# Kernel tuning notes

Hardware: AMD Instinct MI355X
Metric: run time of the kernel (lower is better)

Reference implementation:

```python
import jax, jax.numpy as jnp
import numpy as np
import math

D = 768      # embedding_dim
H = 12       # attn_n_heads
HD = D // H  # head_dim = 64
F = 3072     # ff_latent_dim
B, S = 1, 4096
EPS = 1e-5


def setup_inputs() -> dict:
    key = jax.random.key(0)
    ks = jax.random.split(key, 16)
    s = 0.02
    return {
        "x": jax.random.normal(ks[0], (B, S, D), jnp.float32),
        # per-head Q/K/V projections stacked: [H, D, HD]
        "Wq": jax.random.normal(ks[1], (H, D, HD), jnp.float32) * s,
        "bq": jnp.zeros((H, HD), jnp.float32),
        "Wk": jax.random.normal(ks[2], (H, D, HD), jnp.float32) * s,
        "bk": jnp.zeros((H, HD), jnp.float32),
        "Wv": jax.random.normal(ks[3], (H, D, HD), jnp.float32) * s,
        "bv": jnp.zeros((H, HD), jnp.float32),
        "Wo": jax.random.normal(ks[4], (D, D), jnp.float32) * s,
        "bo": jnp.zeros((D,), jnp.float32),
        "ln1_w": jnp.ones((D,), jnp.float32),
        "ln1_b": jnp.zeros((D,), jnp.float32),
        "ln2_w": jnp.ones((D,), jnp.float32),
        "ln2_b": jnp.zeros((D,), jnp.float32),
        "W1": jax.random.normal(ks[5], (D, F), jnp.float32) * s,
        "b1": jnp.zeros((F,), jnp.float32),
        "W2": jax.random.normal(ks[6], (F, D), jnp.float32) * s,
        "b2": jnp.zeros((D,), jnp.float32),
    }


def _layer_norm(z, w, b):
    mu = jnp.mean(z, axis=-1, keepdims=True)
    var = jnp.mean(jnp.square(z - mu), axis=-1, keepdims=True)
    return (z - mu) * jax.lax.rsqrt(var + EPS) * w + b


def reference(x, Wq, bq, Wk, bk, Wv, bv, Wo, bo,
              ln1_w, ln1_b, ln2_w, ln2_b, W1, b1, W2, b2):
    # pre-norm attention block
    y = _layer_norm(x, ln1_w, ln1_b)
    q = jnp.einsum('bsd,hde->bhse', y, Wq) + bq[None, :, None, :]
    k = jnp.einsum('bsd,hde->bhse', y, Wk) + bk[None, :, None, :]
    v = jnp.einsum('bsd,hde->bhse', y, Wv) + bv[None, :, None, :]
    scores = jnp.einsum('bhqe,bhke->bhqk', q, k) * (1.0 / math.sqrt(HD))
    attn = jax.nn.softmax(scores, axis=-1)            # [B,H,S,S]
    o = jnp.einsum('bhqk,bhke->bhqe', attn, v)        # [B,H,S,HD]
    o = o.transpose(0, 2, 1, 3).reshape(x.shape[0], x.shape[1], D)  # concat heads
    o = o @ Wo + bo
    x = x + o
    # pre-norm FFN block (eval mode: dropout is identity)
    y = _layer_norm(x, ln2_w, ln2_b)
    h = jax.nn.gelu(y @ W1 + b1, approximate=False)   # torch F.gelu default = exact erf
    x = x + (h @ W2 + b2)
    return x
```

## Files before the change

### kernel.cpp

```cpp
#include <hip/hip_runtime.h>
#include <stdint.h>

typedef __bf16 bf16;
typedef __bf16 bf16x2 __attribute__((ext_vector_type(2)));
typedef __bf16 bf16x4 __attribute__((ext_vector_type(4)));
typedef __bf16 bf16x8 __attribute__((ext_vector_type(8)));
typedef float f32x4 __attribute__((ext_vector_type(4)));
typedef float f32x16 __attribute__((ext_vector_type(16)));
typedef uint32_t u32;
typedef unsigned int u32x2 __attribute__((ext_vector_type(2)));

#define QSCALE 0.1803368801111137f

__device__ __forceinline__ float fast_exp2(float x) {
#if __has_builtin(__builtin_amdgcn_exp2f)
  return __builtin_amdgcn_exp2f(x);
#else
  return exp2f(x);
#endif
}

__device__ __forceinline__ float fast_rcp(float x) {
#if __has_builtin(__builtin_amdgcn_rcpf)
  return __builtin_amdgcn_rcpf(x);
#else
  return 1.0f / x;
#endif
}

__device__ __forceinline__ float fast_gelu(float v) {
  float u = v * 0.70710678118654752f;
  float a = __builtin_fabsf(u);
  float t = fast_rcp(__builtin_fmaf(0.47047f, a, 1.0f));
  float e = fast_exp2(-a * a * 1.4426950408889634f);
  float poly = ((0.7478556f * t - 0.0958798f) * t + 0.3480242f) * t;
  float erf_abs = __builtin_fmaf(-poly, e, 1.0f);
  float erf = __builtin_copysignf(erf_abs, u);
  return 0.5f * v * (1.0f + erf);
}

__device__ __forceinline__ u32 pack_bf16(float a, float b) {
  bf16x2 v; v[0] = (bf16)a; v[1] = (bf16)b;
  return __builtin_bit_cast(u32, v);
}

__device__ __forceinline__ void permswap32(u32& a, u32& b) {
#if __has_builtin(__builtin_amdgcn_permlane32_swap)
  u32x2 r = __builtin_amdgcn_permlane32_swap(a, b, false, false);
  a = r[0]; b = r[1];
#else
  asm volatile("v_permlane32_swap_b32 %0, %1" : "+v"(a), "+v"(b));
#endif
}

__device__ __forceinline__ void async16(void* lds, const void* g) {
  __builtin_amdgcn_global_load_lds(
      (__attribute__((address_space(1))) uint32_t*)(uintptr_t)g,
      (__attribute__((address_space(3))) uint32_t*)(uint32_t)(uintptr_t)lds,
      16, 0, 0);
}

__device__ __forceinline__ void transpose_body(
    const float* __restrict__ in, bf16* __restrict__ outp, int R, int C,
    int bx, int by, float (*tile)[33], int t)
{
  int bc = bx * 32, br = by * 32;
  int tc = t & 31, tr = t >> 5;
  #pragma unroll
  for (int i = 0; i < 4; i++)
    tile[tr + i * 8][tc] = in[(size_t)(br + tr + i * 8) * C + bc + tc];
  __syncthreads();
  #pragma unroll
  for (int i = 0; i < 4; i++) {
    int c = bc + tr + i * 8;
    outp[(size_t)c * R + br + tc] = (bf16)tile[tc][tr + i * 8];
  }
}

__global__ __launch_bounds__(256) void prep_kernel(
    const float* __restrict__ x,
    const float* __restrict__ ln1w, const float* __restrict__ ln1b,
    const float* __restrict__ Wq, const float* __restrict__ Wk,
    const float* __restrict__ Wv,
    const float* __restrict__ Wo, const float* __restrict__ W1,
    const float* __restrict__ W2,
    const float* __restrict__ bq, const float* __restrict__ bk,
    const float* __restrict__ bv,
    bf16* __restrict__ ybuf, bf16* __restrict__ Wqkv_t,
    bf16* __restrict__ Wo_t, bf16* __restrict__ W1_t, bf16* __restrict__ W2_t,
    float* __restrict__ bqkv)
{
  __shared__ float tile[32][33];
  int n = blockIdx.x;
  int t = threadIdx.x;
  if (n < 4096) {
    int row = n;
    const float* xr = x + (size_t)row * 768;
    float v0 = xr[t], v1 = xr[t + 256], v2 = xr[t + 512];
    float s = v0 + v1 + v2, s2 = v0 * v0 + v1 * v1 + v2 * v2;
    #pragma unroll
    for (int d = 1; d < 64; d <<= 1) {
      s  += __shfl_xor(s, d, 64);
      s2 += __shfl_xor(s2, d, 64);
    }
    float* red = &tile[0][0];
    int wv = t >> 6, ln = t & 63;
    if (ln == 0) { red[wv] = s; red[4 + wv] = s2; }
    __syncthreads();
    s  = red[0] + red[1] + red[2] + red[3];
    s2 = red[4] + red[5] + red[6] + red[7];
    float mu = s * (1.0f / 768.0f);
    float var = s2 * (1.0f / 768.0f) - mu * mu;
    float rstd = rsqrtf(var + 1e-5f);
    bf16* yr = ybuf + (size_t)row * 768;
    yr[t]       = (bf16)((v0 - mu) * rstd * ln1w[t]       + ln1b[t]);
    yr[t + 256] = (bf16)((v1 - mu) * rstd * ln1w[t + 256] + ln1b[t + 256]);
    yr[t + 512] = (bf16)((v2 - mu) * rstd * ln1w[t + 512] + ln1b[t + 512]);
  } else if (n < 5824) {
    int n2 = n - 4096;
    int bz = n2 / 48, rem = n2 - bz * 48;
    int by = rem / 24, bx = rem - by * 24;
    int part = bz / 12, h = bz - part * 12;
    const float* W = (part == 0) ? Wq : (part == 1) ? Wk : Wv;
    float sc = (part == 0) ? QSCALE : 1.0f;
    int bd = bx * 32, be = by * 32;
    int tc = t & 31, tr = t >> 5;
    #pragma unroll
    for (int i = 0; i < 4; i++)
      tile[tr + i * 8][tc] = W[((size_t)h * 768 + bd + tr + i * 8) * 64 + be + tc] * sc;
    __syncthreads();
    #pragma unroll
    for (int i = 0; i < 4; i++) {
      int e = be + tr + i * 8;
      Wqkv_t[(size_t)(part * 768 + h * 64 + e) * 768 + bd + tc] = (bf16)tile[tc][tr + i * 8];
    }
  } else if (n < 6400) {
    int m = n - 5824;
    transpose_body(Wo, Wo_t, 768, 768, m % 24, m / 24, tile, t);
  } else if (n < 8704) {
    int m = n - 6400;
    transpose_body(W1, W1_t, 768, 3072, m % 96, m / 96, tile, t);
  } else if (n < 11008) {
    int m = n - 8704;
    transpose_body(W2, W2_t, 3072, 768, m % 24, m / 24, tile, t);
  } else {
    int idx = (n - 11008) * 256 + t;
    int part = idx / 768, nn = idx - part * 768;
    const float* B = (part == 0) ? bq : (part == 1) ? bk : bv;
    float v = B[nn];
    if (part == 0) v *= QSCALE;
    bqkv[idx] = v;
  }
}

__global__ __launch_bounds__(256) void reduce_add2_kernel(
    float* __restrict__ out, const bf16* __restrict__ p1,
    const bf16* __restrict__ p2)
{
  int i = blockIdx.x * 256 + threadIdx.x;
  float4 o = ((float4*)out)[i];
  bf16x4 a = ((const bf16x4*)p1)[i];
  bf16x4 b = ((const bf16x4*)p2)[i];
  o.x += (float)a[0] + (float)b[0];
  o.y += (float)a[1] + (float)b[1];
  o.z += (float)a[2] + (float)b[2];
  o.w += (float)a[3] + (float)b[3];
  ((float4*)out)[i] = o;
}

__global__ __launch_bounds__(256) void ln_add_kernel(
    float* __restrict__ x1, const bf16* __restrict__ p,
    const float* __restrict__ w, const float* __restrict__ b,
    bf16* __restrict__ y)
{
  int row = blockIdx.x;
  float* xr = x1 + (size_t)row * 768;
  const bf16* pr = p + (size_t)row * 768;
  int t = threadIdx.x;
  float v0 = xr[t]       + (float)pr[t];
  float v1 = xr[t + 256] + (float)pr[t + 256];
  float v2 = xr[t + 512] + (float)pr[t + 512];
  xr[t] = v0; xr[t + 256] = v1; xr[t + 512] = v2;
  float s = v0 + v1 + v2, s2 = v0 * v0 + v1 * v1 + v2 * v2;
  #pragma unroll
  for (int d = 1; d < 64; d <<= 1) {
    s  += __shfl_xor(s, d, 64);
    s2 += __shfl_xor(s2, d, 64);
  }
  __shared__ float red[8];
  int wv = t >> 6, ln = t & 63;
  if (ln == 0) { red[wv] = s; red[4 + wv] = s2; }
  __syncthreads();
  s  = red[0] + red[1] + red[2] + red[3];
  s2 = red[4] + red[5] + red[6] + red[7];
  float mu = s * (1.0f / 768.0f);
  float var = s2 * (1.0f / 768.0f) - mu * mu;
  float rstd = rsqrtf(var + 1e-5f);
  bf16* yr = y + (size_t)row * 768;
  yr[t]       = (bf16)((v0 - mu) * rstd * w[t]       + b[t]);
  yr[t + 256] = (bf16)((v1 - mu) * rstd * w[t + 256] + b[t + 256]);
  yr[t + 512] = (bf16)((v2 - mu) * rstd * w[t + 512] + b[t + 512]);
}

template <int MODE>
__global__ __launch_bounds__(256) void gemm_bt(
    const bf16* __restrict__ A, const bf16* __restrict__ Bt,
    const float* __restrict__ bias, const float* __restrict__ res,
    void* __restrict__ outp, void* __restrict__ out2, int M, int N, int K)
{
  __shared__ bf16 As[2 * 128 * 32];
  __shared__ bf16 Bs[2 * 128 * 32];
  int t = threadIdx.x;
  int w = t >> 6, lane = t & 63;
  int quad = lane >> 4, l16 = lane & 15;
  int tile_m = blockIdx.y * 128, tile_n = blockIdx.x * 128;

  int srow = lane >> 2;
  int skb = (lane & 3) * 8;
  const bf16* Ag = A  + (size_t)(tile_m + w * 16 + srow) * K + skb;
  const bf16* Bg = Bt + (size_t)(tile_n + w * 16 + srow) * K + skb;
  char* AsB = (char*)As + w * 1024;
  char* BsB = (char*)Bs + w * 1024;
  size_t rstep = (size_t)64 * K;

  int wm = (w >> 1) * 64, wn = (w & 1) * 64;
  f32x4 acc[4][4] = {};

  int kbeg = 0, kend = K;
  if (MODE == 5) {
    int slice = K / (int)gridDim.z;
    kbeg = blockIdx.z * slice;
    kend = kbeg + slice;
  }

  async16(AsB,        Ag + kbeg);
  async16(AsB + 4096, Ag + rstep + kbeg);
  async16(BsB,        Bg + kbeg);
  async16(BsB + 4096, Bg + rstep + kbeg);

  int cur = 0;
  for (int k0 = kbeg; k0 < kend; k0 += 32) {
    __syncthreads();
    if (k0 + 32 < kend) {
      char* An = AsB + (cur ^ 1) * 8192;
      char* Bn = BsB + (cur ^ 1) * 8192;
      async16(An,        Ag + k0 + 32);
      async16(An + 4096, Ag + rstep + k0 + 32);
      async16(Bn,        Bg + k0 + 32);
      async16(Bn + 4096, Bg + rstep + k0 + 32);
    }
    const bf16* Ab = As + cur * 4096;
    const bf16* Bb = Bs + cur * 4096;

    bf16x8 af[4], bfr[4];
    #pragma unroll
    for (int mb = 0; mb < 4; mb++)
      af[mb] = *(const bf16x8*)(Ab + (wm + mb * 16 + l16) * 32 + quad * 8);
    #pragma unroll
    for (int nb = 0; nb < 4; nb++)
      bfr[nb] = *(const bf16x8*)(Bb + (wn + nb * 16 + l16) * 32 + quad * 8);
    #pragma unroll
    for (int mb = 0; mb < 4; mb++)
      #pragma unroll
      for (int nb = 0; nb < 4; nb++)
        acc[mb][nb] = __builtin_amdgcn_mfma_f32_16x16x32_bf16(
            af[mb], bfr[nb], acc[mb][nb], 0, 0, 0);
    cur ^= 1;
  }

  #pragma unroll
  for (int mb = 0; mb < 4; mb++) {
    #pragma unroll
    for (int nb = 0; nb < 4; nb++) {
      int col = tile_n + wn + nb * 16 + l16;
      int row0 = tile_m + wm + mb * 16 + quad * 4;
      if (MODE == 4) {
        float bc = bias[col];
        if (col < 1536) {
          #pragma unroll
          for (int r = 0; r < 4; r++)
            ((bf16*)outp)[(size_t)(row0 + r) * 1536 + col] =
                (bf16)(acc[mb][nb][r] + bc);
        } else {
          bf16x4 pk;
          #pragma unroll
          for (int r = 0; r < 4; r++) pk[r] = (bf16)(acc[mb][nb][r] + bc);
          *(bf16x4*)((bf16*)out2 + (size_t)(col - 1536) * 4096 + row0) = pk;
        }
      } else if (MODE == 2) {
        float bc = bias[col];
        #pragma unroll
        for (int r = 0; r < 4; r++) {
          size_t idx = (size_t)(row0 + r) * N + col;
          ((bf16*)outp)[idx] = (bf16)fast_gelu(acc[mb][nb][r] + bc);
        }
      } else {
        if (blockIdx.z == 0) {
          float bc = bias[col];
          #pragma unroll
          for (int r = 0; r < 4; r++) {
            size_t idx = (size_t)(row0 + r) * N + col;
            ((float*)outp)[idx] = res[idx] + acc[mb][nb][r] + bc;
          }
        } else {
          size_t pbase = (size_t)(blockIdx.z - 1) * M * N;
          #pragma unroll
          for (int r = 0; r < 4; r++) {
            size_t idx = (size_t)(row0 + r) * N + col;
            ((bf16*)out2)[pbase + idx] = (bf16)acc[mb][nb][r];
          }
        }
      }
    }
  }
}

__global__ __launch_bounds__(256) void flash_kernel(
    const bf16* __restrict__ qk, const bf16* __restrict__ vtg,
    bf16* __restrict__ Opart, float* __restrict__ Lpart)
{
  __shared__ char smem[49152];
  bf16* Qs = (bf16*)smem;
  int t = threadIdx.x, w = t >> 6, lane = t & 63;
  int l32 = lane & 31, hi = lane >> 5;
  int qt = blockIdx.x, h = blockIdx.y, z = blockIdx.z;
  int q0 = qt * 128, kv0 = z * 2048;
  int qsel = w & 1, ksel = w >> 1;
  int qw = qsel * 64, kb = ksel * 32;

  int srow = lane >> 3, scol = ((lane & 7) ^ srow) * 8;

  #pragma unroll
  for (int c = 0; c < 4; c++) {
    const bf16* qg = qk + (size_t)(q0 + c * 32 + w * 8 + srow) * 1536 + h * 64 + scol;
    async16(smem + c * 4096 + w * 1024, qg);
  }

  const bf16* kg = qk + 768 + h * 64 + (size_t)(kv0 + w * 8 + srow) * 1536 + scol;
  const bf16* vg = vtg + (size_t)(h * 64 + w * 8 + srow) * 4096 + kv0 + scol;

  {
    char* kb0 = smem + 16384 + w * 1024;
    char* vb0 = smem + 32768 + w * 1024;
    async16(kb0,        kg);
    async16(kb0 + 4096, kg + (size_t)32 * 1536);
    async16(vb0,        vg);
    async16(vb0 + 4096, vg + (size_t)32 * 4096);
  }
  __syncthreads();

  int qr0 = qw + l32, qr1 = qw + 32 + l32;
  bf16x8 qf0[4], qf1[4];
  #pragma unroll
  for (int ks = 0; ks < 4; ks++) {
    qf0[ks] = *(const bf16x8*)(Qs + qr0 * 64 + (((ks * 2 + hi) ^ (qr0 & 7)) * 8));
    qf1[ks] = *(const bf16x8*)(Qs + qr1 * 64 + (((ks * 2 + hi) ^ (qr1 & 7)) * 8));
  }

  f32x16 oT00 = {}, oT10 = {}, oT01 = {}, oT11 = {};
  float l0 = 0.0f, l1 = 0.0f;
  int krow = kb + l32;
  int er0 = l32, er1 = 32 + l32;

  for (int j = 0; j < 32; j++) {
    int cur = j & 1;
    if (j < 31) {
      const bf16* kgn = kg + (size_t)(j + 1) * 64 * 1536;
      const bf16* vgn = vg + (j + 1) * 64;
      char* kbn = smem + 16384 + (cur ^ 1) * 8192 + w * 1024;
      char* vbn = smem + 32768 + (cur ^ 1) * 8192 + w * 1024;
      async16(kbn,        kgn);
      async16(kbn + 4096, kgn + (size_t)32 * 1536);
      async16(vbn,        vgn);
      async16(vbn + 4096, vgn + (size_t)32 * 4096);
    }
    const bf16* Ks = (const bf16*)(smem + 16384 + cur * 8192);
    const bf16* Vs = (const bf16*)(smem + 32768 + cur * 8192);

    f32x16 s0 = {}, s1 = {};
    __builtin_amdgcn_s_setprio(1);
    #pragma unroll
    for (int ks = 0; ks < 4; ks++) {
      bf16x8 kf = *(const bf16x8*)(Ks + krow * 64 + (((ks * 2 + hi) ^ (krow & 7)) * 8));
      s0 = __builtin_amdgcn_mfma_f32_32x32x16_bf16(kf, qf0[ks], s0, 0, 0, 0);
      s1 = __builtin_amdgcn_mfma_f32_32x32x16_bf16(kf, qf1[ks], s1, 0, 0, 0);
    }
    __builtin_amdgcn_s_setprio(0);

    bf16x8 pf00, pf01, pf10, pf11;
    {
      float p[16];
      #pragma unroll
      for (int i = 0; i < 16; i++) p[i] = fast_exp2(s0[i]);
      float t0 = (p[0] + p[1]) + (p[2] + p[3]);
      float t1 = (p[4] + p[5]) + (p[6] + p[7]);
      float t2 = (p[8] + p[9]) + (p[10] + p[11]);
      float t3 = (p[12] + p[13]) + (p[14] + p[15]);
      l0 += (t0 + t1) + (t2 + t3);
      u32 dd[8];
      #pragma unroll
      for (int k = 0; k < 8; k++) dd[k] = pack_bf16(p[2 * k], p[2 * k + 1]);
      permswap32(dd[0], dd[2]);
      permswap32(dd[1], dd[3]);
      permswap32(dd[4], dd[6]);
      permswap32(dd[5], dd[7]);
      pf00 = __builtin_bit_cast(bf16x8, uint4{dd[0], dd[1], dd[2], dd[3]});
      pf01 = __builtin_bit_cast(bf16x8, uint4{dd[4], dd[5], dd[6], dd[7]});
    }
    {
      float p[16];
      #pragma unroll
      for (int i = 0; i < 16; i++) p[i] = fast_exp2(s1[i]);
      float t0 = (p[0] + p[1]) + (p[2] + p[3]);
      float t1 = (p[4] + p[5]) + (p[6] + p[7]);
      float t2 = (p[8] + p[9]) + (p[10] + p[11]);
      float t3 = (p[12] + p[13]) + (p[14] + p[15]);
      l1 += (t0 + t1) + (t2 + t3);
      u32 dd[8];
      #pragma unroll
      for (int k = 0; k < 8; k++) dd[k] = pack_bf16(p[2 * k], p[2 * k + 1]);
      permswap32(dd[0], dd[2]);
      permswap32(dd[1], dd[3]);
      permswap32(dd[4], dd[6]);
      permswap32(dd[5], dd[7]);
      pf10 = __builtin_bit_cast(bf16x8, uint4{dd[0], dd[1], dd[2], dd[3]});
      pf11 = __builtin_bit_cast(bf16x8, uint4{dd[4], dd[5], dd[6], dd[7]});
    }

    __builtin_amdgcn_s_setprio(1);
    #pragma unroll
    for (int kstep = 0; kstep < 2; kstep++) {
      int grp = (kb >> 3) + kstep * 2 + hi;
      bf16x8 va = *(const bf16x8*)(Vs + er0 * 64 + ((grp ^ (er0 & 7)) * 8));
      bf16x8 vb = *(const bf16x8*)(Vs + er1 * 64 + ((grp ^ (er1 & 7)) * 8));
      bf16x8 pa = kstep ? pf01 : pf00;
      bf16x8 pb = kstep ? pf11 : pf10;
      oT00 = __builtin_amdgcn_mfma_f32_32x32x16_bf16(va, pa, oT00, 0, 0, 0);
      oT10 = __builtin_amdgcn_mfma_f32_32x32x16_bf16(vb, pa, oT10, 0, 0, 0);
      oT01 = __builtin_amdgcn_mfma_f32_32x32x16_bf16(va, pb, oT01, 0, 0, 0);
      oT11 = __builtin_amdgcn_mfma_f32_32x32x16_bf16(vb, pb, oT11, 0, 0, 0);
    }
    __builtin_amdgcn_s_setprio(0);

    __syncthreads();
  }

  float lq0 = l0 + __shfl_xor(l0, 32, 64);
  float lq1 = l1 + __shfl_xor(l1, 32, 64);
  float* OS = (float*)smem;
  float* LS = (float*)(smem + 34304);
  if (ksel == 1) {
    #pragma unroll
    for (int i = 0; i < 16; i++) {
      int eoff = (i & 3) + 8 * (i >> 2) + 4 * hi;
      OS[qr0 * 67 + eoff]      = oT00[i];
      OS[qr0 * 67 + 32 + eoff] = oT10[i];
      OS[qr1 * 67 + eoff]      = oT01[i];
      OS[qr1 * 67 + 32 + eoff] = oT11[i];
    }
    if (hi == 0) { LS[qr0] = lq0; LS[qr1] = lq1; }
  }
  __syncthreads();
  if (ksel == 0) {
    size_t tb = ((size_t)z * 12 + h) * 32 + qt;
    float la0 = lq0 + LS[qr0], la1 = lq1 + LS[qr1];
    if (hi == 0) { Lpart[tb * 128 + qr0] = la0; Lpart[tb * 128 + qr1] = la1; }
    bf16* ob0 = Opart + tb * 8192 + (size_t)qr0 * 64;
    bf16* ob1 = Opart + tb * 8192 + (size_t)qr1 * 64;
    #pragma unroll
    for (int g = 0; g < 4; g++) {
      int e0 = 8 * g + 4 * hi;
      bf16x4 a0, a1, b0, b1;
      #pragma unroll
      for (int r = 0; r < 4; r++) {
        a0[r] = (bf16)(oT00[g * 4 + r] + OS[qr0 * 67 + e0 + r]);
        a1[r] = (bf16)(oT10[g * 4 + r] + OS[qr0 * 67 + 32 + e0 + r]);
        b0[r] = (bf16)(oT01[g * 4 + r] + OS[qr1 * 67 + e0 + r]);
        b1[r] = (bf16)(oT11[g * 4 + r] + OS[qr1 * 67 + 32 + e0 + r]);
      }
      *(bf16x4*)(ob0 + e0)      = a0;
      *(bf16x4*)(ob0 + 32 + e0) = a1;
      *(bf16x4*)(ob1 + e0)      = b0;
      *(bf16x4*)(ob1 + 32 + e0) = b1;
    }
  }
}

__global__ __launch_bounds__(256) void flash_combine_kernel(
    const bf16* __restrict__ Opart, const float* __restrict__ Lpart,
    bf16* __restrict__ o)
{
  int qt = blockIdx.x, h = blockIdx.y;
  int t = threadIdx.x;
  size_t t0 = (size_t)h * 32 + qt;
  size_t t1 = (size_t)(12 + h) * 32 + qt;
  #pragma unroll
  for (int qq = 0; qq < 2; qq++) {
    int q = qq * 64 + (t >> 2), eg = (t & 3) * 16;
    float inv = 1.0f / (Lpart[t0 * 128 + q] + Lpart[t1 * 128 + q]);
    const bf16* p0 = Opart + t0 * 8192 + (size_t)q * 64 + eg;
    const bf16* p1 = Opart + t1 * 8192 + (size_t)q * 64 + eg;
    bf16x8 a0 = *(const bf16x8*)p0, a1 = *(const bf16x8*)(p0 + 8);
    bf16x8 b0 = *(const bf16x8*)p1, b1 = *(const bf16x8*)(p1 + 8);
    bf16x8 r0, r1;
    #pragma unroll
    for (int i = 0; i < 8; i++) {
      r0[i] = (bf16)(((float)a0[i] + (float)b0[i]) * inv);
      r1[i] = (bf16)(((float)a1[i] + (float)b1[i]) * inv);
    }
    bf16* op = o + (size_t)(qt * 128 + q) * 768 + h * 64 + eg;
    *(bf16x8*)op       = r0;
    *(bf16x8*)(op + 8) = r1;
  }
}

extern "C" void kernel_launch(void* const* d_in, const int* in_sizes, int n_in,
                              void* d_out, int out_size, void* d_ws, size_t ws_size,
                              hipStream_t stream) {
  const float* x    = (const float*)d_in[0];
  const float* Wq   = (const float*)d_in[1];
  const float* bq   = (const float*)d_in[2];
  const float* Wk   = (const float*)d_in[3];
  const float* bk   = (const float*)d_in[4];
  const float* Wv   = (const float*)d_in[5];
  const float* bv   = (const float*)d_in[6];
  const float* Wo   = (const float*)d_in[7];
  const float* bo   = (const float*)d_in[8];
  const float* ln1w = (const float*)d_in[9];
  const float* ln1b = (const float*)d_in[10];
  const float* ln2w = (const float*)d_in[11];
  const float* ln2b = (const float*)d_in[12];
  const float* W1   = (const float*)d_in[13];
  const float* b1   = (const float*)d_in[14];
  const float* W2   = (const float*)d_in[15];
  const float* b2   = (const float*)d_in[16];
  float* out = (float*)d_out;

  char* ws = (char*)d_ws;
  bf16*  hbuf   = (bf16*)(ws + 0);
  float* Lpart  = (float*)(ws + 0);
  bf16*  ybuf   = (bf16*)(ws + 0);
  bf16*  qkbuf  = (bf16*)(ws + 6291456);
  bf16*  opar_o = (bf16*)(ws + 6291456);
  bf16*  vtg    = (bf16*)(ws + 18874368);
  float* x1     = (float*)(ws + 25165824);
  bf16*  Opart  = (bf16*)(ws + 25165824);
  bf16*  obuf   = (bf16*)(ws + 37748736);
  bf16*  y2buf  = obuf;
  bf16*  opar_f = obuf;
  bf16*  Wqkv_t = (bf16*)(ws + 44040192);
  bf16*  Wo_t   = (bf16*)(ws + 47579136);
  bf16*  W1_t   = (bf16*)(ws + 48758784);
  bf16*  W2_t   = (bf16*)(ws + 53477376);
  float* bqkv   = (float*)(ws + 58195968);

  prep_kernel<<<11017, 256, 0, stream>>>(x, ln1w, ln1b, Wq, Wk, Wv, Wo, W1, W2,
                                         bq, bk, bv,
                                         ybuf, Wqkv_t, Wo_t, W1_t, W2_t, bqkv);
  gemm_bt<4><<<dim3(18, 32), 256, 0, stream>>>(ybuf, Wqkv_t, bqkv,
                                               (const float*)nullptr, qkbuf, vtg,
                                               4096, 2304, 768);
  flash_kernel<<<dim3(32, 12, 2), 256, 0, stream>>>(qkbuf, vtg, Opart, Lpart);
  flash_combine_kernel<<<dim3(32, 12), 256, 0, stream>>>(Opart, Lpart, obuf);
  gemm_bt<5><<<dim3(6, 32, 2), 256, 0, stream>>>(obuf, Wo_t, bo, x, x1, opar_o,
                                                 4096, 768, 768);
  ln_add_kernel<<<4096, 256, 0, stream>>>(x1, opar_o, ln2w, ln2b, y2buf);
  gemm_bt<2><<<dim3(24, 32), 256, 0, stream>>>(y2buf, W1_t, b1,
                                               (const float*)nullptr, hbuf, nullptr,
                                               4096, 3072, 768);
  gemm_bt<5><<<dim3(6, 32, 3), 256, 0, stream>>>(hbuf, W2_t, b2, x1, out, opar_f,
                                                 4096, 768, 3072);
  reduce_add2_kernel<<<3072, 256, 0, stream>>>(out, opar_f,
                                               (const bf16*)(ws + 44040192));
}
```

Baseline: 315.2 us.

## Split flash attention KV into three chunks and halve shared memory

Result: no change. 313.9 us (-0.4%).

```diff
diff --git a/kernel.cpp b/kernel.cpp
--- a/kernel.cpp
+++ b/kernel.cpp
@@ -153,18 +153,14 @@
   }
 }
 
-__global__ __launch_bounds__(256) void reduce_add2_kernel(
-    float* __restrict__ out, const bf16* __restrict__ p1,
-    const bf16* __restrict__ p2)
+__global__ __launch_bounds__(256) void reduce_add_kernel(
+    float* __restrict__ out, const bf16* __restrict__ p)
 {
   int i = blockIdx.x * 256 + threadIdx.x;
   float4 o = ((float4*)out)[i];
-  bf16x4 a = ((const bf16x4*)p1)[i];
-  bf16x4 b = ((const bf16x4*)p2)[i];
-  o.x += (float)a[0] + (float)b[0];
-  o.y += (float)a[1] + (float)b[1];
-  o.z += (float)a[2] + (float)b[2];
-  o.w += (float)a[3] + (float)b[3];
+  bf16x4 v = ((const bf16x4*)p)[i];
+  o.x += (float)v[0]; o.y += (float)v[1];
+  o.z += (float)v[2]; o.w += (float)v[3];
   ((float4*)out)[i] = o;
 }
 
@@ -317,14 +313,15 @@
 
 __global__ __launch_bounds__(256) void flash_kernel(
     const bf16* __restrict__ qk, const bf16* __restrict__ vtg,
-    bf16* __restrict__ Opart, float* __restrict__ Lpart)
+    bf16* __restrict__ Op0, bf16* __restrict__ Op12, float* __restrict__ Lpart)
 {
-  __shared__ char smem[49152];
-  bf16* Qs = (bf16*)smem;
+  __shared__ char smem[32768];
   int t = threadIdx.x, w = t >> 6, lane = t & 63;
   int l32 = lane & 31, hi = lane >> 5;
   int qt = blockIdx.x, h = blockIdx.y, z = blockIdx.z;
-  int q0 = qt * 128, kv0 = z * 2048;
+  int q0 = qt * 128;
+  int nt  = (z == 0) ? 22 : 21;
+  int kv0 = (z == 0) ? 0 : (22 + (z - 1) * 21) * 64;
   int qsel = w & 1, ksel = w >> 1;
   int qw = qsel * 64, kb = ksel * 32;
 
@@ -333,15 +330,16 @@
   #pragma unroll
   for (int c = 0; c < 4; c++) {
     const bf16* qg = qk + (size_t)(q0 + c * 32 + w * 8 + srow) * 1536 + h * 64 + scol;
-    async16(smem + c * 4096 + w * 1024, qg);
+    int base = (c < 2) ? (8192 + c * 4096) : (24576 + (c - 2) * 4096);
+    async16(smem + base + w * 1024, qg);
   }
 
   const bf16* kg = qk + 768 + h * 64 + (size_t)(kv0 + w * 8 + srow) * 1536 + scol;
   const bf16* vg = vtg + (size_t)(h * 64 + w * 8 + srow) * 4096 + kv0 + scol;
 
   {
-    char* kb0 = smem + 16384 + w * 1024;
-    char* vb0 = smem + 32768 + w * 1024;
+    char* kb0 = smem + w * 1024;
+    char* vb0 = smem + 16384 + w * 1024;
     async16(kb0,        kg);
     async16(kb0 + 4096, kg + (size_t)32 * 1536);
     async16(vb0,        vg);
@@ -350,32 +348,35 @@
   __syncthreads();
 
   int qr0 = qw + l32, qr1 = qw + 32 + l32;
+  const bf16* Qbase = (const bf16*)(smem + (qsel ? 24576 : 8192));
+  int r0q = qr0 & 63, r1q = qr1 & 63;
   bf16x8 qf0[4], qf1[4];
   #pragma unroll
   for (int ks = 0; ks < 4; ks++) {
-    qf0[ks] = *(const bf16x8*)(Qs + qr0 * 64 + (((ks * 2 + hi) ^ (qr0 & 7)) * 8));
-    qf1[ks] = *(const bf16x8*)(Qs + qr1 * 64 + (((ks * 2 + hi) ^ (qr1 & 7)) * 8));
-  }
+    qf0[ks] = *(const bf16x8*)(Qbase + r0q * 64 + (((ks * 2 + hi) ^ (r0q & 7)) * 8));
+    qf1[ks] = *(const bf16x8*)(Qbase + r1q * 64 + (((ks * 2 + hi) ^ (r1q & 7)) * 8));
+  }
+  __syncthreads();
 
   f32x16 oT00 = {}, oT10 = {}, oT01 = {}, oT11 = {};
   float l0 = 0.0f, l1 = 0.0f;
   int krow = kb + l32;
   int er0 = l32, er1 = 32 + l32;
 
-  for (int j = 0; j < 32; j++) {
+  for (int j = 0; j < nt; j++) {
     int cur = j & 1;
-    if (j < 31) {
+    if (j < nt - 1) {
       const bf16* kgn = kg + (size_t)(j + 1) * 64 * 1536;
       const bf16* vgn = vg + (j + 1) * 64;
-      char* kbn = smem + 16384 + (cur ^ 1) * 8192 + w * 1024;
-      char* vbn = smem + 32768 + (cur ^ 1) * 8192 + w * 1024;
+      char* kbn = smem + (cur ^ 1) * 8192 + w * 1024;
+      char* vbn = smem + 16384 + (cur ^ 1) * 8192 + w * 1024;
       async16(kbn,        kgn);
       async16(kbn + 4096, kgn + (size_t)32 * 1536);
       async16(vbn,        vgn);
       async16(vbn + 4096, vgn + (size_t)32 * 4096);
     }
-    const bf16* Ks = (const bf16*)(smem + 16384 + cur * 8192);
-    const bf16* Vs = (const bf16*)(smem + 32768 + cur * 8192);
+    const bf16* Ks = (const bf16*)(smem + cur * 8192);
+    const bf16* Vs = (const bf16*)(smem + 16384 + cur * 8192);
 
     f32x16 s0 = {}, s1 = {};
     __builtin_amdgcn_s_setprio(1);
@@ -448,65 +449,94 @@
   float lq0 = l0 + __shfl_xor(l0, 32, 64);
   float lq1 = l1 + __shfl_xor(l1, 32, 64);
   float* OS = (float*)smem;
-  float* LS = (float*)(smem + 34304);
+  float* LS = (float*)(smem + 16896);
+  size_t tb = ((size_t)z * 12 + h) * 32 + qt;
+  bf16* Ob = (z == 0) ? (Op0 + tb * 8192) : (Op12 + (tb - 384) * 8192);
+
   if (ksel == 1) {
     #pragma unroll
     for (int i = 0; i < 16; i++) {
       int eoff = (i & 3) + 8 * (i >> 2) + 4 * hi;
-      OS[qr0 * 67 + eoff]      = oT00[i];
-      OS[qr0 * 67 + 32 + eoff] = oT10[i];
-      OS[qr1 * 67 + eoff]      = oT01[i];
-      OS[qr1 * 67 + 32 + eoff] = oT11[i];
+      OS[qr0 * 33 + eoff] = oT00[i];
+      OS[qr1 * 33 + eoff] = oT01[i];
     }
     if (hi == 0) { LS[qr0] = lq0; LS[qr1] = lq1; }
   }
   __syncthreads();
   if (ksel == 0) {
-    size_t tb = ((size_t)z * 12 + h) * 32 + qt;
     float la0 = lq0 + LS[qr0], la1 = lq1 + LS[qr1];
     if (hi == 0) { Lpart[tb * 128 + qr0] = la0; Lpart[tb * 128 + qr1] = la1; }
-    bf16* ob0 = Opart + tb * 8192 + (size_t)qr0 * 64;
-    bf16* ob1 = Opart + tb * 8192 + (size_t)qr1 * 64;
+    bf16* ob0 = Ob + (size_t)qr0 * 64;
+    bf16* ob1 = Ob + (size_t)qr1 * 64;
     #pragma unroll
     for (int g = 0; g < 4; g++) {
       int e0 = 8 * g + 4 * hi;
-      bf16x4 a0, a1, b0, b1;
+      bf16x4 a0, b0;
       #pragma unroll
       for (int r = 0; r < 4; r++) {
-        a0[r] = (bf16)(oT00[g * 4 + r] + OS[qr0 * 67 + e0 + r]);
-        a1[r] = (bf16)(oT10[g * 4 + r] + OS[qr0 * 67 + 32 + e0 + r]);
-        b0[r] = (bf16)(oT01[g * 4 + r] + OS[qr1 * 67 + e0 + r]);
-        b1[r] = (bf16)(oT11[g * 4 + r] + OS[qr1 * 67 + 32 + e0 + r]);
+        a0[r] = (bf16)(oT00[g * 4 + r] + OS[qr0 * 33 + e0 + r]);
+        b0[r] = (bf16)(oT01[g * 4 + r] + OS[qr1 * 33 + e0 + r]);
       }
-      *(bf16x4*)(ob0 + e0)      = a0;
+      *(bf16x4*)(ob0 + e0) = a0;
+      *(bf16x4*)(ob1 + e0) = b0;
+    }
+  }
+  __syncthreads();
+  if (ksel == 1) {
+    #pragma unroll
+    for (int i = 0; i < 16; i++) {
+      int eoff = (i & 3) + 8 * (i >> 2) + 4 * hi;
+      OS[qr0 * 33 + eoff] = oT10[i];
+      OS[qr1 * 33 + eoff] = oT11[i];
+    }
+  }
+  __syncthreads();
+  if (ksel == 0) {
+    bf16* ob0 = Ob + (size_t)qr0 * 64;
+    bf16* ob1 = Ob + (size_t)qr1 * 64;
+    #pragma unroll
+    for (int g = 0; g < 4; g++) {
+      int e0 = 8 * g + 4 * hi;
+      bf16x4 a1, b1;
+      #pragma unroll
+      for (int r = 0; r < 4; r++) {
+        a1[r] = (bf16)(oT10[g * 4 + r] + OS[qr0 * 33 + e0 + r]);
+        b1[r] = (bf16)(oT11[g * 4 + r] + OS[qr1 * 33 + e0 + r]);
+      }
       *(bf16x4*)(ob0 + 32 + e0) = a1;
-      *(bf16x4*)(ob1 + e0)      = b0;
       *(bf16x4*)(ob1 + 32 + e0) = b1;
     }
   }
 }
 
 __global__ __launch_bounds__(256) void flash_combine_kernel(
-    const bf16* __restrict__ Opart, const float* __restrict__ Lpart,
-    bf16* __restrict__ o)
+    const bf16* __restrict__ Op0, const bf16* __restrict__ Op12,
+    const float* __restrict__ Lpart, bf16* __restrict__ o)
 {
   int qt = blockIdx.x, h = blockIdx.y;
   int t = threadIdx.x;
-  size_t t0 = (size_t)h * 32 + qt;
-  size_t t1 = (size_t)(12 + h) * 32 + qt;
+  size_t b0 = (size_t)h * 32 + qt;
+  size_t b1 = (size_t)h * 32 + qt;
+  size_t b2 = (size_t)(12 + h) * 32 + qt;
+  size_t lt0 = (size_t)h * 32 + qt;
+  size_t lt1 = (size_t)(12 + h) * 32 + qt;
+  size_t lt2 = (size_t)(24 + h) * 32 + qt;
   #pragma unroll
   for (int qq = 0; qq < 2; qq++) {
     int q = qq * 64 + (t >> 2), eg = (t & 3) * 16;
-    float inv = 1.0f / (Lpart[t0 * 128 + q] + Lpart[t1 * 128 + q]);
-    const bf16* p0 = Opart + t0 * 8192 + (size_t)q * 64 + eg;
-    const bf16* p1 = Opart + t1 * 8192 + (size_t)q * 64 + eg;
-    bf16x8 a0 = *(const bf16x8*)p0, a1 = *(const bf16x8*)(p0 + 8);
-    bf16x8 b0 = *(const bf16x8*)p1, b1 = *(const bf16x8*)(p1 + 8);
+    float inv = 1.0f / (Lpart[lt0 * 128 + q] + Lpart[lt1 * 128 + q] +
+                        Lpart[lt2 * 128 + q]);
+    const bf16* p0 = Op0  + b0 * 8192 + (size_t)q * 64 + eg;
+    const bf16* p1 = Op12 + b1 * 8192 + (size_t)q * 64 + eg;
+    const bf16* p2 = Op12 + b2 * 8192 + (size_t)q * 64 + eg;
+    bf16x8 x0 = *(const bf16x8*)p0, x1 = *(const bf16x8*)(p0 + 8);
+    bf16x8 y0 = *(const bf16x8*)p1, y1 = *(const bf16x8*)(p1 + 8);
+    bf16x8 z0 = *(const bf16x8*)p2, z1 = *(const bf16x8*)(p2 + 8);
     bf16x8 r0, r1;
     #pragma unroll
     for (int i = 0; i < 8; i++) {
-      r0[i] = (bf16)(((float)a0[i] + (float)b0[i]) * inv);
-      r1[i] = (bf16)(((float)a1[i] + (float)b1[i]) * inv);
+      r0[i] = (bf16)(((float)x0[i] + (float)y0[i] + (float)z0[i]) * inv);
+      r1[i] = (bf16)(((float)x1[i] + (float)y1[i] + (float)z1[i]) * inv);
     }
     bf16* op = o + (size_t)(qt * 128 + q) * 768 + h * 64 + eg;
     *(bf16x8*)op       = r0;
@@ -538,13 +568,13 @@
 
   char* ws = (char*)d_ws;
   bf16*  hbuf   = (bf16*)(ws + 0);
-  float* Lpart  = (float*)(ws + 0);
   bf16*  ybuf   = (bf16*)(ws + 0);
+  bf16*  Op0    = (bf16*)(ws + 0);
   bf16*  qkbuf  = (bf16*)(ws + 6291456);
   bf16*  opar_o = (bf16*)(ws + 6291456);
   bf16*  vtg    = (bf16*)(ws + 18874368);
   float* x1     = (float*)(ws + 25165824);
-  bf16*  Opart  = (bf16*)(ws + 25165824);
+  bf16*  Op12   = (bf16*)(ws + 25165824);
   bf16*  obuf   = (bf16*)(ws + 37748736);
   bf16*  y2buf  = obuf;
   bf16*  opar_f = obuf;
@@ -552,6 +582,7 @@
   bf16*  Wo_t   = (bf16*)(ws + 47579136);
   bf16*  W1_t   = (bf16*)(ws + 48758784);
   bf16*  W2_t   = (bf16*)(ws + 53477376);
+  float* LpartN = (float*)(ws + 44040192);
   float* bqkv   = (float*)(ws + 58195968);
 
   prep_kernel<<<11017, 256, 0, stream>>>(x, ln1w, ln1b, Wq, Wk, Wv, Wo, W1, W2,
@@ -560,16 +591,15 @@
   gemm_bt<4><<<dim3(18, 32), 256, 0, stream>>>(ybuf, Wqkv_t, bqkv,
                                                (const float*)nullptr, qkbuf, vtg,
                                                4096, 2304, 768);
-  flash_kernel<<<dim3(32, 12, 2), 256, 0, stream>>>(qkbuf, vtg, Opart, Lpart);
-  flash_combine_kernel<<<dim3(32, 12), 256, 0, stream>>>(Opart, Lpart, obuf);
+  flash_kernel<<<dim3(32, 12, 3), 256, 0, stream>>>(qkbuf, vtg, Op0, Op12, LpartN);
+  flash_combine_kernel<<<dim3(32, 12), 256, 0, stream>>>(Op0, Op12, LpartN, obuf);
   gemm_bt<5><<<dim3(6, 32, 2), 256, 0, stream>>>(obuf, Wo_t, bo, x, x1, opar_o,
                                                  4096, 768, 768);
   ln_add_kernel<<<4096, 256, 0, stream>>>(x1, opar_o, ln2w, ln2b, y2buf);
   gemm_bt<2><<<dim3(24, 32), 256, 0, stream>>>(y2buf, W1_t, b1,
                                                (const float*)nullptr, hbuf, nullptr,
                                                4096, 3072, 768);
-  gemm_bt<5><<<dim3(6, 32, 3), 256, 0, stream>>>(hbuf, W2_t, b2, x1, out, opar_f,
+  gemm_bt<5><<<dim3(6, 32, 2), 256, 0, stream>>>(hbuf, W2_t, b2, x1, out, opar_f,
                                                  4096, 768, 3072);
-  reduce_add2_kernel<<<3072, 256, 0, stream>>>(out, opar_f,
-                                               (const bf16*)(ws + 44040192));
-}
+  reduce_add_kernel<<<3072, 256, 0, stream>>>(out, opar_f);
+}
```
